# Performance work log

Measured on AMD Instinct MI355X. Metric: run time of the kernel, lower is better.

Reference implementation:

```python
import jax, jax.numpy as jnp
import numpy as np

TOP_K = 2


def setup_inputs() -> dict:
    key = jax.random.key(0)
    k0, k1, k2, k3, k4, k5 = jax.random.split(key, 6)
    N, D_IN, D_OUT, H, G = 8192, 1024, 1024, 4096, 3
    E = 2 ** G
    x = jax.random.normal(k0, (N, D_IN), jnp.float32)
    # gate: Linear(in_dim, gate_dim, bias=False) followed by act (ReLU)
    Wg = jax.random.normal(k1, (D_IN, G), jnp.float32) * (1.0 / np.sqrt(D_IN))
    # experts: per-expert 2-layer MLP: Linear(in,hid) + ReLU + Linear(hid,out)
    W1 = jax.random.normal(k2, (E, D_IN, H), jnp.float32) * (1.0 / np.sqrt(D_IN))
    b1 = jax.random.normal(k3, (E, H), jnp.float32) * 0.01
    W2 = jax.random.normal(k4, (E, H, D_OUT), jnp.float32) * (1.0 / np.sqrt(H))
    b2 = jax.random.normal(k5, (E, D_OUT), jnp.float32) * 0.01
    return {"x": x, "Wg": Wg, "W1": W1, "b1": b1, "W2": W2, "b2": b2}


def _hypercube_mask(E, G, dtype):
    # binary(arange(2^G), G) * 2 - 1 : corners of the hypercube in {-1,+1}^G
    codes = jnp.arange(E)
    bits = (codes[:, None] >> jnp.arange(G)[None, :]) & 1  # [E, G]
    return (bits * 2 - 1).astype(dtype)


def reference(x, Wg, W1, b1, W2, b2):
    G = Wg.shape[1]
    E = W1.shape[0]
    N = x.shape[0]
    mask = _hypercube_mask(E, G, x.dtype)                 # [E, G]
    logits = jax.nn.relu(x @ Wg)                          # [N, G]
    scores = logits @ mask.T                              # [N, E] = sum_d logits*mask
    probs = jax.nn.softmax(scores, axis=1)                # softmax over experts
    topv, topi = jax.lax.top_k(probs, TOP_K)              # [N, k]
    topv = topv / topv.sum(axis=-1, keepdims=True)        # renormalize selected probs
    # dense combine weights: zero for non-selected experts (same math as gather/scatter dispatch)
    combine = jnp.zeros((N, E), x.dtype).at[jnp.arange(N)[:, None], topi].set(topv)
    out = jnp.zeros((N, W2.shape[2]), x.dtype)
    for e in range(E):  # small fixed expert count
        h = jax.nn.relu(x @ W1[e] + b1[e])                # [N, H]
        out = out + combine[:, e:e + 1] * (h @ W2[e] + b2[e])
    return out
```

## Files before the change

### kernel.cpp

```cpp
#include <hip/hip_runtime.h>

#define NTOK 8192
#define DIN  1024
#define DOUT 1024
#define HDIM 4096
#define NEXP 8
#define NPAIR (NTOK * 2)

typedef __attribute__((ext_vector_type(8))) short bf16x8;
typedef __attribute__((ext_vector_type(4))) float f32x4;

__device__ __forceinline__ unsigned short f2bf(float f) {
  union { float f; unsigned u; } v; v.f = f;
  unsigned u = v.u;
  unsigned r = (u + 0x7fffu + ((u >> 16) & 1u)) >> 16;
  return (unsigned short)r;
}

__device__ __forceinline__ void gload16(const void* g, void* l) {
  __builtin_amdgcn_global_load_lds(
      (const __attribute__((address_space(1))) unsigned int*)g,
      (__attribute__((address_space(3))) unsigned int*)l, 16, 0, 0);
}

__global__ void gate_kernel(const float* __restrict__ x, const float* __restrict__ Wg,
                            int* __restrict__ cnt, int* __restrict__ ptok,
                            float* __restrict__ pw) {
  const int lane = threadIdx.x & 63;
  const int t = blockIdx.x * 4 + (threadIdx.x >> 6);
  const float* xr = x + (size_t)t * DIN + lane * 16;
  const float* wr = Wg + (size_t)lane * 16 * 3;
  double d0 = 0, d1 = 0, d2 = 0;
#pragma unroll
  for (int j = 0; j < 16; j++) {
    double xv = xr[j];
    d0 += xv * wr[j * 3 + 0];
    d1 += xv * wr[j * 3 + 1];
    d2 += xv * wr[j * 3 + 2];
  }
#pragma unroll
  for (int o = 32; o > 0; o >>= 1) {
    d0 += __shfl_down(d0, o);
    d1 += __shfl_down(d1, o);
    d2 += __shfl_down(d2, o);
  }
  if (lane == 0) {
    double l0 = d0 > 0 ? d0 : 0, l1 = d1 > 0 ? d1 : 0, l2 = d2 > 0 ? d2 : 0;
    double s[NEXP];
#pragma unroll
    for (int e = 0; e < NEXP; e++)
      s[e] = ((e & 1) ? l0 : -l0) + ((e & 2) ? l1 : -l1) + ((e & 4) ? l2 : -l2);
    int e0 = 0;
    for (int e = 1; e < NEXP; e++) if (s[e] > s[e0]) e0 = e;
    int e1 = -1;
    for (int e = 0; e < NEXP; e++) { if (e == e0) continue; if (e1 < 0 || s[e] > s[e1]) e1 = e; }
    double w0 = 1.0 / (1.0 + exp(s[e1] - s[e0]));
    double w1 = 1.0 - w0;
    int p0 = atomicAdd(cnt + e0, 1);
    ptok[e0 * NTOK + p0] = t; pw[e0 * NTOK + p0] = (float)w0;
    int p1 = atomicAdd(cnt + e1, 1);
    ptok[e1 * NTOK + p1] = t; pw[e1 * NTOK + p1] = (float)w1;
  }
}

__global__ void scan_kernel(const int* __restrict__ cnt, int* __restrict__ off) {
  if (threadIdx.x == 0) {
    int a = 0;
    for (int e = 0; e < NEXP; e++) { off[e] = a; a += cnt[e]; }
  }
}

__global__ void cvt_bf16_kernel(const float* __restrict__ src,
                                unsigned short* __restrict__ dst, int n) {
  int i = (blockIdx.x * 256 + threadIdx.x) * 8;
  if (i >= n) return;
  float4 a = *(const float4*)(src + i);
  float4 b = *(const float4*)(src + i + 4);
  __align__(16) unsigned short t[8] = {f2bf(a.x), f2bf(a.y), f2bf(a.z), f2bf(a.w),
                                       f2bf(b.x), f2bf(b.y), f2bf(b.z), f2bf(b.w)};
  *(uint4*)(dst + i) = *(const uint4*)t;
}

__global__ void transpose_cvt(const float* __restrict__ src,
                              unsigned short* __restrict__ dst, int K, int N) {
  __shared__ float tile[64][65];
  const size_t base = (size_t)blockIdx.z * K * N;
  const float* s = src + base;
  unsigned short* d = dst + base;
  int n0 = blockIdx.x * 64, k0 = blockIdx.y * 64;
  for (int idx = threadIdx.x; idx < 64 * 16; idx += 256) {
    int r = idx >> 4, c4 = (idx & 15) * 4;
    float4 v = *(const float4*)(s + (size_t)(k0 + r) * N + n0 + c4);
    tile[r][c4 + 0] = v.x; tile[r][c4 + 1] = v.y;
    tile[r][c4 + 2] = v.z; tile[r][c4 + 3] = v.w;
  }
  __syncthreads();
  for (int idx = threadIdx.x; idx < 64 * 8; idx += 256) {
    int nl = idx >> 3, c8 = (idx & 7) * 8;
    __align__(16) unsigned short tmp[8];
#pragma unroll
    for (int j = 0; j < 8; j++) tmp[j] = f2bf(tile[c8 + j][nl]);
    *(uint4*)(d + (size_t)(n0 + nl) * K + k0 + c8) = *(const uint4*)tmp;
  }
}


#define RD_A(qm, bufb)                                                         \
  _Pragma("unroll") for (int fi = 0; fi < 4; fi++)                             \
    _Pragma("unroll") for (int ks = 0; ks < 2; ks++)                           \
      areg[fi][ks] = *(const bf16x8*)(lds + (bufb) +                           \
          (unsigned)((rowA_base + (qm) * 64 + fi * 16) * 128 +                 \
                     ((ks * 64 + hi * 16) ^ cxor)));

#define RD_B(qn, breg, bufb)                                                   \
  _Pragma("unroll") for (int fj = 0; fj < 2; fj++)                             \
    _Pragma("unroll") for (int ks = 0; ks < 2; ks++)                           \
      breg[fj][ks] = *(const bf16x8*)(lds + (bufb) + 32768u +                  \
          (unsigned)((rowB_base + (qn) * 32 + fj * 16) * 128 +                 \
                     ((ks * 64 + hi * 16) ^ cxor)));

#define MM_Q(qm, qn, breg)                                                     \
  _Pragma("unroll") for (int fi = 0; fi < 4; fi++)                             \
    _Pragma("unroll") for (int fj = 0; fj < 2; fj++)                           \
      _Pragma("unroll") for (int ks = 0; ks < 2; ks++)                         \
        acc[(qm) * 4 + fi][(qn) * 2 + fj] =                                    \
            __builtin_amdgcn_mfma_f32_16x16x32_bf16(                           \
                areg[fi][ks], breg[fj][ks], acc[(qm) * 4 + fi][(qn) * 2 + fj], \
                0, 0, 0);

#define STG(hh, bv, kel)                                                       \
  do {                                                                         \
    unsigned db = (unsigned)(bv) * 65536u +                                    \
                  (((hh) < 2) ? (unsigned)(hh) * 16384u                        \
                              : 32768u + (unsigned)((hh) - 2) * 16384u);       \
    const unsigned short* s0 = ((hh) < 2) ? aptr[(hh) * 2] : bptr[((hh) - 2) * 2];         \
    const unsigned short* s1 = ((hh) < 2) ? aptr[(hh) * 2 + 1] : bptr[((hh) - 2) * 2 + 1]; \
    gload16(s0 + (kel), lds + db + (unsigned)tid * 16u);                       \
    gload16(s1 + (kel), lds + db + 8192u + (unsigned)tid * 16u);               \
  } while (0)

#define PH_TOP(hh)                                                             \
  if (more) STG(hh, bufn, kel);

#define PH_MFMA(qm, qn, breg)                                                  \
  __builtin_amdgcn_s_barrier();                                                \
  __builtin_amdgcn_sched_barrier(0);                                           \
  __builtin_amdgcn_s_setprio(1);                                               \
  MM_Q(qm, qn, breg);                                                          \
  __builtin_amdgcn_s_setprio(0);                                               \
  __builtin_amdgcn_sched_barrier(0);

__global__ __launch_bounds__(512, 1) void gemm1_kernel(
    const unsigned short* __restrict__ xbf,
    const unsigned short* __restrict__ w1t,
    const float* __restrict__ b1,
    const int* __restrict__ cnt, const int* __restrict__ off,
    const int* __restrict__ ptok,
    unsigned short* __restrict__ h)
{
  extern __shared__ char lds[];
  const int bid = blockIdx.x;
  const int e = bid & 7;
  const int ce = cnt[e];
  const int idx = bid >> 3;
  const int mt = idx >> 4;
  const int nt = idx & 15;
  const int m0 = mt * 256;
  if (m0 >= ce) return;
  const int n0 = nt * 256;
  const int oe = off[e];
  const int tid = threadIdx.x;
  const int lane = tid & 63;
  const int wid = tid >> 6;
  const int wm = wid >> 2;
  const int wn = wid & 3;

  const int kofs = ((tid & 7) * 8) ^ (((tid >> 3) & 7) << 3);
  const int rth = tid >> 3;
  const unsigned short* aptr[4];
  const unsigned short* bptr[4];
  const unsigned short* wb = w1t + (size_t)e * HDIM * DIN;
#pragma unroll
  for (int i = 0; i < 4; i++) {
    int r = rth + i * 64;
    int ta = ptok[e * NTOK + min(m0 + r, ce - 1)];
    aptr[i] = xbf + (size_t)ta * DIN + kofs;
    bptr[i] = wb + (size_t)(n0 + r) * DIN + kofs;
  }

  const int fr = lane & 15;
  const int hi = lane >> 4;
  const int cxor = (fr & 7) << 4;
  const int rowA_base = wm * 128 + fr;
  const int rowB_base = wn * 64 + fr;

  f32x4 acc[8][4] = {};
  bf16x8 areg[4][2], b0reg[2][2], b1reg[2][2];

  {
    const bool more = true; const int bufn = 0; const int kel = 0;
    PH_TOP(0); PH_TOP(1); PH_TOP(2); PH_TOP(3);
  }

  const int KT = DIN / 64;
  for (int t = 0; t < KT; t++) {
    const unsigned bb = (unsigned)(t & 1) * 65536u;
    const int bufn = (t + 1) & 1;
    const int kel = (t + 1) * 64;
    const bool more = (t + 1 < KT);
    PH_TOP(0);
    if (more) asm volatile("s_waitcnt vmcnt(2)" ::: "memory");
    else      asm volatile("s_waitcnt vmcnt(0)" ::: "memory");
    __builtin_amdgcn_s_barrier();
    __builtin_amdgcn_sched_barrier(0);
    RD_A(0, bb); RD_B(0, b0reg, bb); RD_B(1, b1reg, bb);
    __builtin_amdgcn_sched_barrier(0);
    __builtin_amdgcn_s_setprio(1);
    MM_Q(0, 0, b0reg);
    __builtin_amdgcn_s_setprio(0);
    __builtin_amdgcn_sched_barrier(0);
    __builtin_amdgcn_s_barrier();
    PH_TOP(1);
    PH_MFMA(0, 1, b1reg);
    RD_A(1, bb);
    __builtin_amdgcn_sched_barrier(0);
    __builtin_amdgcn_s_barrier();
    PH_TOP(2);
    PH_MFMA(1, 1, b1reg);
    __builtin_amdgcn_s_barrier();
    PH_TOP(3);
    PH_MFMA(1, 0, b0reg);
    __builtin_amdgcn_s_barrier();
  }

#pragma unroll
  for (int am = 0; am < 8; am++) {
    int rbase = wm * 128 + am * 16 + hi * 4;
#pragma unroll
    for (int r = 0; r < 4; r++) {
      int grow = m0 + rbase + r;
      if (grow >= ce) continue;
      size_t hoff = (size_t)(oe + grow) * HDIM;
#pragma unroll
      for (int an = 0; an < 4; an++) {
        int col = n0 + wn * 64 + an * 16 + fr;
        float v = acc[am][an][r] + b1[e * HDIM + col];
        h[hoff + col] = f2bf(v > 0.f ? v : 0.f);
      }
    }
  }
}

__global__ __launch_bounds__(512, 1) void gemm2_kernel(
    const unsigned short* __restrict__ h,
    const unsigned short* __restrict__ w2t,
    const float* __restrict__ b2,
    const int* __restrict__ cnt, const int* __restrict__ off,
    const int* __restrict__ ptok, const float* __restrict__ pw,
    float* __restrict__ out)
{
  extern __shared__ char lds[];
  const int bid = blockIdx.x;
  const int e = bid & 7;
  const int ce = cnt[e];
  const int idx = bid >> 3;
  const int mt = idx >> 2;
  const int nt = idx & 3;
  const int m0 = mt * 256;
  if (m0 >= ce) return;
  const int n0 = nt * 256;
  const int oe = off[e];
  const int tid = threadIdx.x;
  const int lane = tid & 63;
  const int wid = tid >> 6;
  const int wm = wid >> 2;
  const int wn = wid & 3;

  const int kofs = ((tid & 7) * 8) ^ (((tid >> 3) & 7) << 3);
  const int rth = tid >> 3;
  const unsigned short* aptr[4];
  const unsigned short* bptr[4];
  const unsigned short* wb = w2t + (size_t)e * DOUT * HDIM;
#pragma unroll
  for (int i = 0; i < 4; i++) {
    int r = rth + i * 64;
    int rc = min(m0 + r, ce - 1);
    aptr[i] = h + (size_t)(oe + rc) * HDIM + kofs;
    bptr[i] = wb + (size_t)(n0 + r) * HDIM + kofs;
  }

  const int fr = lane & 15;
  const int hi = lane >> 4;
  const int cxor = (fr & 7) << 4;
  const int rowA_base = wm * 128 + fr;
  const int rowB_base = wn * 64 + fr;

  f32x4 acc[8][4] = {};
  bf16x8 areg[4][2], b0reg[2][2], b1reg[2][2];

  {
    const bool more = true; const int bufn = 0; const int kel = 0;
    PH_TOP(0); PH_TOP(1); PH_TOP(2); PH_TOP(3);
  }

  const int KT = HDIM / 64;
  for (int t = 0; t < KT; t++) {
    const unsigned bb = (unsigned)(t & 1) * 65536u;
    const int bufn = (t + 1) & 1;
    const int kel = (t + 1) * 64;
    const bool more = (t + 1 < KT);
    PH_TOP(0);
    if (more) asm volatile("s_waitcnt vmcnt(2)" ::: "memory");
    else      asm volatile("s_waitcnt vmcnt(0)" ::: "memory");
    __builtin_amdgcn_s_barrier();
    __builtin_amdgcn_sched_barrier(0);
    RD_A(0, bb); RD_B(0, b0reg, bb); RD_B(1, b1reg, bb);
    __builtin_amdgcn_sched_barrier(0);
    __builtin_amdgcn_s_setprio(1);
    MM_Q(0, 0, b0reg);
    __builtin_amdgcn_s_setprio(0);
    __builtin_amdgcn_sched_barrier(0);
    __builtin_amdgcn_s_barrier();
    PH_TOP(1);
    PH_MFMA(0, 1, b1reg);
    RD_A(1, bb);
    __builtin_amdgcn_sched_barrier(0);
    __builtin_amdgcn_s_barrier();
    PH_TOP(2);
    PH_MFMA(1, 1, b1reg);
    __builtin_amdgcn_s_barrier();
    PH_TOP(3);
    PH_MFMA(1, 0, b0reg);
    __builtin_amdgcn_s_barrier();
  }

#pragma unroll
  for (int am = 0; am < 8; am++) {
    int rbase = wm * 128 + am * 16 + hi * 4;
#pragma unroll
    for (int r = 0; r < 4; r++) {
      int grow = m0 + rbase + r;
      if (grow >= ce) continue;
      int pidx = e * NTOK + grow;
      int token = ptok[pidx];
      float w = pw[pidx];
#pragma unroll
      for (int an = 0; an < 4; an++) {
        int col = n0 + wn * 64 + an * 16 + fr;
        float v = (acc[am][an][r] + b2[e * DOUT + col]) * w;
        atomicAdd(out + (size_t)token * DOUT + col, v);
      }
    }
  }
}

extern "C" void kernel_launch(void* const* d_in, const int* in_sizes, int n_in,
                              void* d_out, int out_size, void* d_ws, size_t ws_size,
                              hipStream_t stream) {
  const float* x  = (const float*)d_in[0];
  const float* Wg = (const float*)d_in[1];
  const float* W1 = (const float*)d_in[2];
  const float* b1 = (const float*)d_in[3];
  const float* W2 = (const float*)d_in[4];
  const float* b2 = (const float*)d_in[5];
  float* out = (float*)d_out;

  char* ws = (char*)d_ws;
  size_t o = 0;
  auto nxt = [&](size_t b) { char* p = ws + o; o = (o + b + 255) & ~(size_t)255; return p; };
  int* cnt = (int*)nxt(64);
  int* off = (int*)nxt(64);
  int* ptok = (int*)nxt((size_t)NEXP * NTOK * 4);
  float* pw = (float*)nxt((size_t)NEXP * NTOK * 4);
  unsigned short* xbf = (unsigned short*)nxt((size_t)NTOK * DIN * 2);
  unsigned short* w1t = (unsigned short*)nxt((size_t)NEXP * HDIM * DIN * 2);
  unsigned short* w2t = (unsigned short*)nxt((size_t)NEXP * DOUT * HDIM * 2);
  unsigned short* hbuf = (unsigned short*)nxt((size_t)NPAIR * HDIM * 2);

  hipFuncSetAttribute((const void*)gemm1_kernel,
                      hipFuncAttributeMaxDynamicSharedMemorySize, 131072);
  hipFuncSetAttribute((const void*)gemm2_kernel,
                      hipFuncAttributeMaxDynamicSharedMemorySize, 131072);

  hipMemsetAsync(cnt, 0, 64, stream);
  hipMemsetAsync(out, 0, (size_t)NTOK * DOUT * 4, stream);

  gate_kernel<<<NTOK / 4, 256, 0, stream>>>(x, Wg, cnt, ptok, pw);
  scan_kernel<<<1, 64, 0, stream>>>(cnt, off);
  cvt_bf16_kernel<<<(NTOK * DIN / 8) / 256, 256, 0, stream>>>(x, xbf, NTOK * DIN);
  transpose_cvt<<<dim3(HDIM / 64, DIN / 64, NEXP), 256, 0, stream>>>(W1, w1t, DIN, HDIM);
  transpose_cvt<<<dim3(DOUT / 64, HDIM / 64, NEXP), 256, 0, stream>>>(W2, w2t, HDIM, DOUT);

  gemm1_kernel<<<8 * (NTOK / 256) * (HDIM / 256), 512, 131072, stream>>>(
      xbf, w1t, b1, cnt, off, ptok, hbuf);
  gemm2_kernel<<<8 * (NTOK / 256) * (DOUT / 256), 512, 131072, stream>>>(
      hbuf, w2t, b2, cnt, off, ptok, pw, out);
}
```

Baseline: 901.3 us.

## Restructure GEMM k-loop with inline-asm LDS reads and single barrier per tile

Replaces the four-barrier-per-iteration phased k-loop in both expert GEMM kernels with a shared KLOOP macro. LDS fragments are read through inline-asm ds_read_b128 with precomputed swizzled offsets, and MFMAs are gated on explicit lgkmcnt waits instead of s_barrier. Global-to-LDS prefetch of the next tile is issued between compute phases, followed by one vmcnt(0) wait and one barrier per iteration. The aim is to cut barrier and synchronisation overhead. The cost is that the full vmcnt(0) drain at the end of every iteration may expose global load latency that the earlier partial wait hid.

```diff
diff --git a/kernel.cpp b/kernel.cpp
--- a/kernel.cpp
+++ b/kernel.cpp
@@ -22,6 +22,17 @@
       (const __attribute__((address_space(1))) unsigned int*)g,
       (__attribute__((address_space(3))) unsigned int*)l, 16, 0, 0);
 }
+
+__device__ __forceinline__ bf16x8 ds_read128(unsigned addr) {
+  bf16x8 r;
+  asm volatile("ds_read_b128 %0, %1" : "=&v"(r) : "v"(addr));
+  return r;
+}
+
+#define LGKM4() asm volatile("s_waitcnt lgkmcnt(4)" ::: "memory")
+#define LGKM0() asm volatile("s_waitcnt lgkmcnt(0)" ::: "memory")
+#define VM0()   asm volatile("s_waitcnt vmcnt(0)" ::: "memory")
+#define SB0()   __builtin_amdgcn_sched_barrier(0)
 
 __global__ void gate_kernel(const float* __restrict__ x, const float* __restrict__ Wg,
                             int* __restrict__ cnt, int* __restrict__ ptok,
@@ -105,29 +116,6 @@
 }
 
 
-#define RD_A(qm, bufb)                                                         \
-  _Pragma("unroll") for (int fi = 0; fi < 4; fi++)                             \
-    _Pragma("unroll") for (int ks = 0; ks < 2; ks++)                           \
-      areg[fi][ks] = *(const bf16x8*)(lds + (bufb) +                           \
-          (unsigned)((rowA_base + (qm) * 64 + fi * 16) * 128 +                 \
-                     ((ks * 64 + hi * 16) ^ cxor)));
-
-#define RD_B(qn, breg, bufb)                                                   \
-  _Pragma("unroll") for (int fj = 0; fj < 2; fj++)                             \
-    _Pragma("unroll") for (int ks = 0; ks < 2; ks++)                           \
-      breg[fj][ks] = *(const bf16x8*)(lds + (bufb) + 32768u +                  \
-          (unsigned)((rowB_base + (qn) * 32 + fj * 16) * 128 +                 \
-                     ((ks * 64 + hi * 16) ^ cxor)));
-
-#define MM_Q(qm, qn, breg)                                                     \
-  _Pragma("unroll") for (int fi = 0; fi < 4; fi++)                             \
-    _Pragma("unroll") for (int fj = 0; fj < 2; fj++)                           \
-      _Pragma("unroll") for (int ks = 0; ks < 2; ks++)                         \
-        acc[(qm) * 4 + fi][(qn) * 2 + fj] =                                    \
-            __builtin_amdgcn_mfma_f32_16x16x32_bf16(                           \
-                areg[fi][ks], breg[fj][ks], acc[(qm) * 4 + fi][(qn) * 2 + fj], \
-                0, 0, 0);
-
 #define STG(hh, bv, kel)                                                       \
   do {                                                                         \
     unsigned db = (unsigned)(bv) * 65536u +                                    \
@@ -139,16 +127,54 @@
     gload16(s1 + (kel), lds + db + 8192u + (unsigned)tid * 16u);               \
   } while (0)
 
-#define PH_TOP(hh)                                                             \
-  if (more) STG(hh, bufn, kel);
-
-#define PH_MFMA(qm, qn, breg)                                                  \
+#define RD_A(qm, bb)                                                           \
+  _Pragma("unroll") for (int fi = 0; fi < 4; fi++) {                           \
+    areg[fi][0] = ds_read128(aoff + (bb) + (qm) * 8192u + fi * 2048u + kx0);   \
+    areg[fi][1] = ds_read128(aoff + (bb) + (qm) * 8192u + fi * 2048u + kx1);   \
+  }
+
+#define RD_B(qn, breg, bb)                                                     \
+  _Pragma("unroll") for (int fj = 0; fj < 2; fj++) {                           \
+    breg[fj][0] = ds_read128(boff + (bb) + (qn) * 4096u + fj * 2048u + kx0);   \
+    breg[fj][1] = ds_read128(boff + (bb) + (qn) * 4096u + fj * 2048u + kx1);   \
+  }
+
+#define MM(qm, qn, breg)                                                       \
+  __builtin_amdgcn_s_setprio(1);                                               \
+  _Pragma("unroll") for (int ks = 0; ks < 2; ks++)                             \
+    _Pragma("unroll") for (int fi = 0; fi < 4; fi++)                           \
+      _Pragma("unroll") for (int fj = 0; fj < 2; fj++)                         \
+        acc[(qm) * 4 + fi][(qn) * 2 + fj] =                                    \
+            __builtin_amdgcn_mfma_f32_16x16x32_bf16(                           \
+                areg[fi][ks], breg[fj][ks], acc[(qm) * 4 + fi][(qn) * 2 + fj], \
+                0, 0, 0);                                                      \
+  __builtin_amdgcn_s_setprio(0);
+
+#define KLOOP(KT)                                                              \
+  STG(0, 0, 0); STG(1, 0, 0); STG(2, 0, 0); STG(3, 0, 0);                      \
+  VM0();                                                                       \
   __builtin_amdgcn_s_barrier();                                                \
-  __builtin_amdgcn_sched_barrier(0);                                           \
-  __builtin_amdgcn_s_setprio(1);                                               \
-  MM_Q(qm, qn, breg);                                                          \
-  __builtin_amdgcn_s_setprio(0);                                               \
-  __builtin_amdgcn_sched_barrier(0);
+  for (int t = 0; t < (KT); t++) {                                             \
+    const unsigned bb = (unsigned)(t & 1) * 65536u;                            \
+    const int bufn = (t + 1) & 1;                                              \
+    const int kel = (t + 1) * 64;                                              \
+    const bool more = (t + 1 < (KT));                                          \
+    RD_A(0, bb);                                                               \
+    RD_B(0, b0reg, bb);                                                        \
+    RD_B(1, b1reg, bb);                                                        \
+    if (more) { STG(0, bufn, kel); STG(1, bufn, kel); }                        \
+    LGKM4(); SB0();                                                            \
+    MM(0, 0, b0reg);                                                           \
+    LGKM0(); SB0();                                                            \
+    MM(0, 1, b1reg);                                                           \
+    RD_A(1, bb);                                                               \
+    if (more) { STG(2, bufn, kel); STG(3, bufn, kel); }                        \
+    LGKM0(); SB0();                                                            \
+    MM(1, 1, b1reg);                                                           \
+    MM(1, 0, b0reg);                                                           \
+    VM0();                                                                     \
+    __builtin_amdgcn_s_barrier();                                              \
+  }
 
 __global__ __launch_bounds__(512, 1) void gemm1_kernel(
     const unsigned short* __restrict__ xbf,
@@ -190,48 +216,17 @@
 
   const int fr = lane & 15;
   const int hi = lane >> 4;
-  const int cxor = (fr & 7) << 4;
-  const int rowA_base = wm * 128 + fr;
-  const int rowB_base = wn * 64 + fr;
+  const unsigned cxor = (unsigned)((fr & 7) << 4);
+  const unsigned ldsbase = (unsigned)(size_t)(void*)lds;
+  const unsigned aoff = ldsbase + (unsigned)((wm * 128 + fr) * 128);
+  const unsigned boff = ldsbase + 32768u + (unsigned)((wn * 64 + fr) * 128);
+  const unsigned kx0 = (unsigned)((hi * 16) ^ cxor);
+  const unsigned kx1 = (unsigned)((64 + hi * 16) ^ cxor);
 
   f32x4 acc[8][4] = {};
   bf16x8 areg[4][2], b0reg[2][2], b1reg[2][2];
 
-  {
-    const bool more = true; const int bufn = 0; const int kel = 0;
-    PH_TOP(0); PH_TOP(1); PH_TOP(2); PH_TOP(3);
-  }
-
-  const int KT = DIN / 64;
-  for (int t = 0; t < KT; t++) {
-    const unsigned bb = (unsigned)(t & 1) * 65536u;
-    const int bufn = (t + 1) & 1;
-    const int kel = (t + 1) * 64;
-    const bool more = (t + 1 < KT);
-    PH_TOP(0);
-    if (more) asm volatile("s_waitcnt vmcnt(2)" ::: "memory");
-    else      asm volatile("s_waitcnt vmcnt(0)" ::: "memory");
-    __builtin_amdgcn_s_barrier();
-    __builtin_amdgcn_sched_barrier(0);
-    RD_A(0, bb); RD_B(0, b0reg, bb); RD_B(1, b1reg, bb);
-    __builtin_amdgcn_sched_barrier(0);
-    __builtin_amdgcn_s_setprio(1);
-    MM_Q(0, 0, b0reg);
-    __builtin_amdgcn_s_setprio(0);
-    __builtin_amdgcn_sched_barrier(0);
-    __builtin_amdgcn_s_barrier();
-    PH_TOP(1);
-    PH_MFMA(0, 1, b1reg);
-    RD_A(1, bb);
-    __builtin_amdgcn_sched_barrier(0);
-    __builtin_amdgcn_s_barrier();
-    PH_TOP(2);
-    PH_MFMA(1, 1, b1reg);
-    __builtin_amdgcn_s_barrier();
-    PH_TOP(3);
-    PH_MFMA(1, 0, b0reg);
-    __builtin_amdgcn_s_barrier();
-  }
+  KLOOP(DIN / 64);
 
 #pragma unroll
   for (int am = 0; am < 8; am++) {
@@ -291,48 +286,17 @@
 
   const int fr = lane & 15;
   const int hi = lane >> 4;
-  const int cxor = (fr & 7) << 4;
-  const int rowA_base = wm * 128 + fr;
-  const int rowB_base = wn * 64 + fr;
+  const unsigned cxor = (unsigned)((fr & 7) << 4);
+  const unsigned ldsbase = (unsigned)(size_t)(void*)lds;
+  const unsigned aoff = ldsbase + (unsigned)((wm * 128 + fr) * 128);
+  const unsigned boff = ldsbase + 32768u + (unsigned)((wn * 64 + fr) * 128);
+  const unsigned kx0 = (unsigned)((hi * 16) ^ cxor);
+  const unsigned kx1 = (unsigned)((64 + hi * 16) ^ cxor);
 
   f32x4 acc[8][4] = {};
   bf16x8 areg[4][2], b0reg[2][2], b1reg[2][2];
 
-  {
-    const bool more = true; const int bufn = 0; const int kel = 0;
-    PH_TOP(0); PH_TOP(1); PH_TOP(2); PH_TOP(3);
-  }
-
-  const int KT = HDIM / 64;
-  for (int t = 0; t < KT; t++) {
-    const unsigned bb = (unsigned)(t & 1) * 65536u;
-    const int bufn = (t + 1) & 1;
-    const int kel = (t + 1) * 64;
-    const bool more = (t + 1 < KT);
-    PH_TOP(0);
-    if (more) asm volatile("s_waitcnt vmcnt(2)" ::: "memory");
-    else      asm volatile("s_waitcnt vmcnt(0)" ::: "memory");
-    __builtin_amdgcn_s_barrier();
-    __builtin_amdgcn_sched_barrier(0);
-    RD_A(0, bb); RD_B(0, b0reg, bb); RD_B(1, b1reg, bb);
-    __builtin_amdgcn_sched_barrier(0);
-    __builtin_amdgcn_s_setprio(1);
-    MM_Q(0, 0, b0reg);
-    __builtin_amdgcn_s_setprio(0);
-    __builtin_amdgcn_sched_barrier(0);
-    __builtin_amdgcn_s_barrier();
-    PH_TOP(1);
-    PH_MFMA(0, 1, b1reg);
-    RD_A(1, bb);
-    __builtin_amdgcn_sched_barrier(0);
-    __builtin_amdgcn_s_barrier();
-    PH_TOP(2);
-    PH_MFMA(1, 1, b1reg);
-    __builtin_amdgcn_s_barrier();
-    PH_TOP(3);
-    PH_MFMA(1, 0, b0reg);
-    __builtin_amdgcn_s_barrier();
-  }
+  KLOOP(HDIM / 64);
 
 #pragma unroll
   for (int am = 0; am < 8; am++) {
```

Measured after the change: 887.4 us. No clear change (-1.5%).
